# Performance work log

Measured on AMD Instinct MI355X. Metric: run time of the kernel, lower is better.

The kernel has to match this reference:

```python
import jax, jax.numpy as jnp
import numpy as np

B, S, H = 2, 512, 768
E, M, R, R2 = 64, 64, 128, 128
NER_C, REL_C, SIZE_E, CLS = 10, 8, 32, 101
NEG = -1e30


def _linear(x, w, b):
    # torch nn.Linear convention: w is [out, in]
    return x @ w.T + b


def _span_pool(emb, masks):
    # emb [B,S,H], masks [B,K,S] -> masked max over tokens -> [B,K,H]
    neg = jnp.where(masks[..., None] != 0, 0.0, NEG)  # [B,K,S,1]
    return jnp.max(neg + emb[:, None, :, :], axis=2)


def _classify_spans(input_ids, emb, masks, size_emb, rep_w, rep_b, head_w, head_b):
    pool = _span_pool(emb, masks)                      # [B,K,H]
    cls_idx = jnp.argmax((input_ids == CLS).astype(jnp.int32), axis=1)
    ctx = emb[jnp.arange(emb.shape[0]), cls_idx]       # [B,H] (get_token)
    rep = jnp.concatenate([jnp.broadcast_to(ctx[:, None, :], pool.shape), pool, size_emb], axis=-1)
    clf = _linear(jax.nn.relu(_linear(rep, rep_w, rep_b)), head_w, head_b)
    return clf, pool


def _classify_relations(pool, size_emb, rels, rel_masks, emb, w1, b1, w2, b2, w3, b3):
    Bc = pool.shape[0]
    bidx = jnp.arange(Bc)[:, None, None]
    pairs = pool[bidx, rels].reshape(Bc, rels.shape[1], -1)        # [B,R,2H]
    size_pairs = size_emb[bidx, rels].reshape(Bc, rels.shape[1], -1)  # [B,R,2*SIZE_E]
    # masked max over context tokens (rel mask)
    ctx = jnp.max(jnp.where(rel_masks[..., None] != 0, 0.0, NEG) + emb[:, None, :, :], axis=2)
    ctx = jnp.where(jnp.any(rel_masks != 0, axis=-1)[..., None], ctx, 0.0)
    rel_repr = jnp.concatenate([ctx, pairs, size_pairs], axis=-1)  # [B,R,3H+2*SIZE_E]
    h = jax.nn.relu(_linear(rel_repr, w1, b1))
    h = jax.nn.relu(_linear(h, w2, b2))
    return _linear(h, w3, b3)


def setup_inputs():
    key = jax.random.key(0)
    ks = jax.random.split(key, 24)
    p = lambda k, shape: jax.random.normal(k, shape, jnp.float32) * 0.02
    ids = jax.random.randint(ks[0], (B, S), 2000, 30000)
    ids = ids.at[:, 0].set(CLS)  # exactly one cls token per row
    return dict(
        input_ids=ids,
        entity_masks=jax.random.randint(ks[1], (B, E, S), 0, 2).astype(jnp.int32),
        entity_sizes=jax.random.randint(ks[2], (B, E), 0, 100),
        mention_masks=jax.random.randint(ks[3], (B, M, S), 0, 2).astype(jnp.int32),
        mention_sizes=jax.random.randint(ks[4], (B, M), 0, 100),
        relations=jax.random.randint(ks[5], (B, R, 2), 0, E),
        rel_masks=jax.random.randint(ks[6], (B, R, S), 0, 2).astype(jnp.int32),
        references=jax.random.randint(ks[7], (B, R2, 2), 0, M),
        references_masks=jax.random.randint(ks[8], (B, R2, S), 0, 2).astype(jnp.int32),
        token_embedding=jax.random.normal(ks[9], (B, S, H), jnp.float32),
        ner_size_emb=p(ks[10], (100, SIZE_E)),
        emd_size_emb=p(ks[11], (100, SIZE_E)),
        ner_rep_w=p(ks[12], (H, 2 * H + SIZE_E)), ner_rep_b=jnp.zeros(H, jnp.float32),
        ner_head_w=p(ks[13], (NER_C, H)), ner_head_b=jnp.zeros(NER_C, jnp.float32),
        emd_rep_w=p(ks[14], (H, 2 * H + SIZE_E)), emd_rep_b=jnp.zeros(H, jnp.float32),
        emd_head_w=p(ks[15], (2, H)), emd_head_b=jnp.zeros(2, jnp.float32),
        rel_w1=p(ks[16], (H, 3 * H + 2 * SIZE_E)), rel_b1=jnp.zeros(H, jnp.float32),
        rel_w2=p(ks[17], (H, H)), rel_b2=jnp.zeros(H, jnp.float32),
        rel_w3=p(ks[18], (REL_C, H)), rel_b3=jnp.zeros(REL_C, jnp.float32),
        cr_w1=p(ks[19], (H, 3 * H + 2 * SIZE_E)), cr_b1=jnp.zeros(H, jnp.float32),
        cr_w2=p(ks[20], (H, H)), cr_b2=jnp.zeros(H, jnp.float32),
        cr_w3=p(ks[21], (1, H)), cr_b3=jnp.zeros(1, jnp.float32),
    )


def reference(input_ids, entity_masks, entity_sizes, mention_masks, mention_sizes,
              relations, rel_masks, references, references_masks, token_embedding,
              ner_size_emb, emd_size_emb,
              ner_rep_w, ner_rep_b, ner_head_w, ner_head_b,
              emd_rep_w, emd_rep_b, emd_head_w, emd_head_b,
              rel_w1, rel_b1, rel_w2, rel_b2, rel_w3, rel_b3,
              cr_w1, cr_b1, cr_w2, cr_b2, cr_w3, cr_b3):
    sz = ner_size_emb[entity_sizes]                                    # [B,E,SIZE_E]
    entity_clf, entity_pool = _classify_spans(input_ids, token_embedding, entity_masks, sz,
                                              ner_rep_w, ner_rep_b, ner_head_w, ner_head_b)
    rel_clf = _classify_relations(entity_pool, sz, relations, rel_masks, token_embedding,
                                  rel_w1, rel_b1, rel_w2, rel_b2, rel_w3, rel_b3)
    msz = emd_size_emb[mention_sizes]
    mention_clf, mention_pool = _classify_spans(input_ids, token_embedding, mention_masks, msz,
                                                emd_rep_w, emd_rep_b, emd_head_w, emd_head_b)
    ref_clf = _classify_relations(mention_pool, msz, references, references_masks, token_embedding,
                                  cr_w1, cr_b1, cr_w2, cr_b2, cr_w3, cr_b3)
    return entity_clf, rel_clf, mention_clf, ref_clf
```

## Files before the change

### kernel.cpp

```cpp
#include <hip/hip_runtime.h>
#include <hip/hip_bf16.h>

typedef __hip_bfloat16 bf16;
typedef __attribute__((ext_vector_type(8))) short short8;
typedef __attribute__((ext_vector_type(4))) float f32x4;

#define SS 512
#define HD 768
#define NSPLIT 8

#define WOFF_NER 0
#define WOFF_EMD 1204224
#define WOFF_RW1 2408448
#define WOFF_CW1 4227072
#define WOFF_RW2 6045696
#define WOFF_CW2 6635520
#define W_TOT    7225344
#define CVT_BLOCKS (W_TOT / 4096)
#define D1_BLOCKS (768 + CVT_BLOCKS + 4)

__global__ __launch_bounds__(256) void k_d1(
    const int* __restrict__ e_masks, const int* __restrict__ m_masks,
    const int* __restrict__ r_masks, const int* __restrict__ c_masks,
    const float* __restrict__ emb, const int* __restrict__ input_ids,
    const int* __restrict__ esizes, const int* __restrict__ msizes,
    const float* __restrict__ nsemb, const float* __restrict__ esemb,
    const float* __restrict__ s0, const float* __restrict__ s1,
    const float* __restrict__ s2, const float* __restrict__ s3,
    const float* __restrict__ s4, const float* __restrict__ s5,
    bf16* __restrict__ wdst, bf16* __restrict__ part, int* __restrict__ flags,
    bf16* __restrict__ sze, bf16* __restrict__ szm,
    bf16* __restrict__ ctxb, float* __restrict__ out)
{
  int bx = blockIdx.x;
  int t  = threadIdx.x;

  if (bx >= 768 + CVT_BLOCKS) {
    int q = bx - (768 + CVT_BLOCKS);
    if (q == 0) {
      for (int i = t; i < 128 * 32; i += 256)
        sze[i] = __hip_bfloat16(nsemb[(size_t)esizes[i >> 5] * 32 + (i & 31)]);
    } else if (q == 1) {
      for (int i = t; i < 128 * 32; i += 256)
        szm[i] = __hip_bfloat16(esemb[(size_t)msizes[i >> 5] * 32 + (i & 31)]);
    } else if (q == 2) {
      __shared__ int s_cls;
      for (int b2 = 0; b2 < 2; b2++) {
        if (t == 0) s_cls = SS;
        __syncthreads();
        for (int s = t; s < SS; s += 256)
          if (input_ids[b2 * SS + s] == 101) atomicMin(&s_cls, s);
        __syncthreads();
        int ci = (s_cls == SS) ? 0 : s_cls;
        for (int hh = t; hh < HD; hh += 256)
          ctxb[(size_t)b2 * HD + hh] = __hip_bfloat16(emb[((size_t)b2 * SS + ci) * HD + hh]);
        __syncthreads();
      }
    } else {
      for (int i = t; i < 3840; i += 256) out[i] = 0.f;
    }
    return;
  }

  if (bx >= 768) {
    size_t i0 = (size_t)(bx - 768) * 4096;
    const float* s; size_t segoff;
    if      (i0 < WOFF_EMD) { s = s0; segoff = 0; }
    else if (i0 < WOFF_RW1) { s = s1; segoff = WOFF_EMD; }
    else if (i0 < WOFF_CW1) { s = s2; segoff = WOFF_RW1; }
    else if (i0 < WOFF_RW2) { s = s3; segoff = WOFF_CW1; }
    else if (i0 < WOFF_CW2) { s = s4; segoff = WOFF_RW2; }
    else                    { s = s5; segoff = WOFF_CW2; }
    #pragma unroll
    for (int j = 0; j < 4; j++) {
      size_t i = i0 + (size_t)j * 1024 + (size_t)t * 4;
      float4 v = *(const float4*)(s + (i - segoff));
      bf16 tmp[4] = { __hip_bfloat16(v.x), __hip_bfloat16(v.y),
                      __hip_bfloat16(v.z), __hip_bfloat16(v.w) };
      *(short4*)(wdst + i) = *(const short4*)tmp;
    }
    return;
  }

  int g  = bx % 48;
  int b  = (bx / 48) & 1;
  int sp = bx / 96;
  int j0 = g * 8;

  const int* marr; int row0;
  if      (j0 < 64)  { marr = e_masks; row0 = b*64  +  j0;        }
  else if (j0 < 128) { marr = m_masks; row0 = b*64  + (j0-64);    }
  else if (j0 < 256) { marr = r_masks; row0 = b*128 + (j0-128);   }
  else               { marr = c_masks; row0 = b*128 + (j0-256);   }

  __shared__ unsigned s_pack[64];
  __shared__ unsigned s_any;
  if (t == 0) s_any = 0u;
  __syncthreads();

  int sbase = sp * 64;
  if (t < 64) {
    unsigned w = 0;
    #pragma unroll
    for (int k = 0; k < 8; k++) {
      int mm = marr[(size_t)(row0 + k) * SS + sbase + t];
      w |= (mm != 0 ? 1u : 0u) << k;
    }
    s_pack[t] = w;
    atomicOr(&s_any, w);
  }
  __syncthreads();

  float acc[8][3];
  #pragma unroll
  for (int k = 0; k < 8; k++)
    #pragma unroll
    for (int i = 0; i < 3; i++) acc[k][i] = -INFINITY;

  const float* ep = emb + ((size_t)b * SS + sbase) * HD + t;
  #pragma unroll 2
  for (int s = 0; s < 64; s++) {
    float v0 = ep[0];
    float v1 = ep[256];
    float v2 = ep[512];
    ep += HD;
    unsigned wm = __builtin_amdgcn_readfirstlane(s_pack[s]);
    #pragma unroll
    for (int k = 0; k < 8; k++) {
      if (wm & (1u << k)) {
        acc[k][0] = fmaxf(acc[k][0], v0);
        acc[k][1] = fmaxf(acc[k][1], v1);
        acc[k][2] = fmaxf(acc[k][2], v2);
      }
    }
  }

  #pragma unroll
  for (int k = 0; k < 8; k++) {
    int sg = b * 384 + j0 + k;
    bf16* dst = part + ((size_t)sp * 768 + sg) * HD;
    dst[t]       = __hip_bfloat16(acc[k][0]);
    dst[t + 256] = __hip_bfloat16(acc[k][1]);
    dst[t + 512] = __hip_bfloat16(acc[k][2]);
  }
  if (t < 8) flags[sp * 768 + b * 384 + j0 + t] = (int)((s_any >> t) & 1u);
}

__global__ __launch_bounds__(256) void k_combine(
    const bf16* __restrict__ part, const int* __restrict__ flags,
    bf16* __restrict__ epool, bf16* __restrict__ mpool,
    bf16* __restrict__ rctx, bf16* __restrict__ cctx)
{
  int sg = blockIdx.x;
  int b = sg / 384, j = sg % 384;
  int any = 0;
  #pragma unroll
  for (int sp = 0; sp < NSPLIT; sp++) any |= flags[sp * 768 + sg];
  #pragma unroll
  for (int i = 0; i < 3; i++) {
    int h = threadIdx.x + i * 256;
    float v = -INFINITY;
    #pragma unroll
    for (int sp = 0; sp < NSPLIT; sp++)
      v = fmaxf(v, (float)part[((size_t)sp * 768 + sg) * HD + h]);
    if      (j < 64)  epool[((size_t)b*64  + j)       * HD + h] = __hip_bfloat16(v);
    else if (j < 128) mpool[((size_t)b*64  + (j-64))  * HD + h] = __hip_bfloat16(v);
    else if (j < 256) rctx [((size_t)b*128 + (j-128)) * HD + h] = __hip_bfloat16(any ? v : 0.f);
    else              cctx [((size_t)b*128 + (j-256)) * HD + h] = __hip_bfloat16(any ? v : 0.f);
  }
}

struct P1 {
  const bf16 *ctx, *pool, *sz; const int* ridx;
  const short* W; const float* bias;
  bf16* C;
  const float *hw, *hb; float* outp;
  int is_rel, N, K, Mtiles;
};
struct P1x4 { P1 p[4]; };

__global__ __launch_bounds__(256, 2) void k_gemm1(P1x4 args)
{
  P1 g = args.p[blockIdx.z];
  int x = blockIdx.x;
  if (x >= g.Mtiles) return;
  int mt = x * 32, nt = blockIdx.y * 32;
  int wave = threadIdx.x >> 6, lane = threadIdx.x & 63;
  int lm = lane & 15, quad = lane >> 4;
  int K_ = g.K;

  const bf16 *g0[2], *g1[2], *g2[2], *g3[2], *g4[2];
  int rr[2] = { mt + lm, mt + 16 + lm };
  #pragma unroll
  for (int i = 0; i < 2; i++) {
    int r = rr[i];
    if (g.is_rel) {
      int b = r >> 7;
      int i0 = g.ridx[2 * r], i1 = g.ridx[2 * r + 1];
      g0[i] = g.ctx  + (size_t)r * HD;
      g1[i] = g.pool + (size_t)(b * 64 + i0) * HD;
      g2[i] = g.pool + (size_t)(b * 64 + i1) * HD;
      g3[i] = g.sz   + (size_t)(b * 64 + i0) * 32;
      g4[i] = g.sz   + (size_t)(b * 64 + i1) * 32;
    } else {
      g0[i] = g.ctx  + (size_t)(r >> 6) * HD;
      g1[i] = g.pool + (size_t)r * HD;
      g2[i] = g.sz   + (size_t)r * 32;
      g3[i] = g2[i]; g4[i] = g2[i];
    }
  }
  const short* w0p = g.W + (size_t)(nt + lm)      * K_ + quad * 8;
  const short* w1p = g.W + (size_t)(nt + 16 + lm) * K_ + quad * 8;

  f32x4 acc00 = {0.f,0.f,0.f,0.f}, acc01 = {0.f,0.f,0.f,0.f};
  f32x4 acc10 = {0.f,0.f,0.f,0.f}, acc11 = {0.f,0.f,0.f,0.f};

  for (int k32 = wave * 32; k32 < K_; k32 += 128) {
    const bf16 *b0, *b1;
    if      (k32 < 768)  { b0 = g0[0] + k32;          b1 = g0[1] + k32;          }
    else if (k32 < 1536) { b0 = g1[0] + (k32 - 768);  b1 = g1[1] + (k32 - 768);  }
    else if (k32 < 2304) { b0 = g2[0] + (k32 - 1536); b1 = g2[1] + (k32 - 1536); }
    else if (k32 < 2336) { b0 = g3[0] + (k32 - 2304); b1 = g3[1] + (k32 - 2304); }
    else                 { b0 = g4[0] + (k32 - 2336); b1 = g4[1] + (k32 - 2336); }
    short8 a0 = *(const short8*)((const short*)b0 + quad * 8);
    short8 a1 = *(const short8*)((const short*)b1 + quad * 8);
    short8 w0 = *(const short8*)(w0p + k32);
    short8 w1 = *(const short8*)(w1p + k32);
    acc00 = __builtin_amdgcn_mfma_f32_16x16x32_bf16(a0, w0, acc00, 0, 0, 0);
    acc01 = __builtin_amdgcn_mfma_f32_16x16x32_bf16(a0, w1, acc01, 0, 0, 0);
    acc10 = __builtin_amdgcn_mfma_f32_16x16x32_bf16(a1, w0, acc10, 0, 0, 0);
    acc11 = __builtin_amdgcn_mfma_f32_16x16x32_bf16(a1, w1, acc11, 0, 0, 0);
  }

  __shared__ float smem[4 * 32 * 32];
  #pragma unroll
  for (int reg = 0; reg < 4; reg++) {
    int r = quad * 4 + reg;
    smem[wave*1024 + r*32 + lm]             = acc00[reg];
    smem[wave*1024 + r*32 + 16 + lm]        = acc01[reg];
    smem[wave*1024 + (16 + r)*32 + lm]      = acc10[reg];
    smem[wave*1024 + (16 + r)*32 + 16 + lm] = acc11[reg];
  }
  __syncthreads();

  int c = threadIdx.x & 31;
  int rb = threadIdx.x >> 5;
  float bb = g.bias[nt + c];
  #pragma unroll
  for (int i = 0; i < 4; i++) {
    int r = rb + 8 * i;
    float v = smem[r*32 + c] + smem[1024 + r*32 + c] + smem[2048 + r*32 + c] + smem[3072 + r*32 + c];
    v = fmaxf(v + bb, 0.f);
    if (g.C) g.C[(size_t)(mt + r) * HD + nt + c] = __hip_bfloat16(v);
    else     smem[r*32 + c] = v;
  }
  __syncthreads();

  if (!g.C) {
    int r = threadIdx.x >> 3, oi = threadIdx.x & 7;
    for (int o = oi; o < g.N; o += 8) {
      float s = 0.f;
      #pragma unroll
      for (int cc = 0; cc < 32; cc++) {
        int c2 = (cc + r) & 31;
        s += smem[r*32 + c2] * g.hw[(size_t)o * HD + nt + c2];
      }
      if (blockIdx.y == 0) s += g.hb[o];
      atomicAdd(g.outp + (size_t)(mt + r) * g.N + o, s);
    }
  }
}

struct P2 { const short* A; const short* W; const float* bias;
            const float *hw, *hb; float* outp; int N; };
struct P2x2 { P2 p[2]; };

__global__ __launch_bounds__(256, 2) void k_gemm2(P2x2 args)
{
  P2 g = args.p[blockIdx.z];
  int mt = blockIdx.x * 32, nt = blockIdx.y * 32;
  int wave = threadIdx.x >> 6, lane = threadIdx.x & 63;
  int lm = lane & 15, quad = lane >> 4;

  const short* a0p = g.A + (size_t)(mt + lm)      * HD + quad * 8;
  const short* a1p = g.A + (size_t)(mt + 16 + lm) * HD + quad * 8;
  const short* w0p = g.W + (size_t)(nt + lm)      * HD + quad * 8;
  const short* w1p = g.W + (size_t)(nt + 16 + lm) * HD + quad * 8;

  f32x4 acc00 = {0.f,0.f,0.f,0.f}, acc01 = {0.f,0.f,0.f,0.f};
  f32x4 acc10 = {0.f,0.f,0.f,0.f}, acc11 = {0.f,0.f,0.f,0.f};

  for (int k32 = wave * 32; k32 < HD; k32 += 128) {
    short8 a0 = *(const short8*)(a0p + k32);
    short8 a1 = *(const short8*)(a1p + k32);
    short8 w0 = *(const short8*)(w0p + k32);
    short8 w1 = *(const short8*)(w1p + k32);
    acc00 = __builtin_amdgcn_mfma_f32_16x16x32_bf16(a0, w0, acc00, 0, 0, 0);
    acc01 = __builtin_amdgcn_mfma_f32_16x16x32_bf16(a0, w1, acc01, 0, 0, 0);
    acc10 = __builtin_amdgcn_mfma_f32_16x16x32_bf16(a1, w0, acc10, 0, 0, 0);
    acc11 = __builtin_amdgcn_mfma_f32_16x16x32_bf16(a1, w1, acc11, 0, 0, 0);
  }

  __shared__ float smem[4 * 32 * 32];
  #pragma unroll
  for (int reg = 0; reg < 4; reg++) {
    int r = quad * 4 + reg;
    smem[wave*1024 + r*32 + lm]             = acc00[reg];
    smem[wave*1024 + r*32 + 16 + lm]        = acc01[reg];
    smem[wave*1024 + (16 + r)*32 + lm]      = acc10[reg];
    smem[wave*1024 + (16 + r)*32 + 16 + lm] = acc11[reg];
  }
  __syncthreads();

  int c = threadIdx.x & 31;
  int rb = threadIdx.x >> 5;
  float bb = g.bias[nt + c];
  #pragma unroll
  for (int i = 0; i < 4; i++) {
    int r = rb + 8 * i;
    float v = smem[r*32 + c] + smem[1024 + r*32 + c] + smem[2048 + r*32 + c] + smem[3072 + r*32 + c];
    smem[r*32 + c] = fmaxf(v + bb, 0.f);
  }
  __syncthreads();

  int r = threadIdx.x >> 3, oi = threadIdx.x & 7;
  for (int o = oi; o < g.N; o += 8) {
    float s = 0.f;
    #pragma unroll
    for (int cc = 0; cc < 32; cc++) {
      int c2 = (cc + r) & 31;
      s += smem[r*32 + c2] * g.hw[(size_t)o * HD + nt + c2];
    }
    if (blockIdx.y == 0) s += g.hb[o];
    atomicAdd(g.outp + (size_t)(mt + r) * g.N + o, s);
  }
}

extern "C" void kernel_launch(void* const* d_in, const int* in_sizes, int n_in,
                              void* d_out, int out_size, void* d_ws, size_t ws_size,
                              hipStream_t stream)
{
  const int*   input_ids  = (const int*)d_in[0];
  const int*   e_masks    = (const int*)d_in[1];
  const int*   e_sizes    = (const int*)d_in[2];
  const int*   m_masks    = (const int*)d_in[3];
  const int*   m_sizes    = (const int*)d_in[4];
  const int*   relations  = (const int*)d_in[5];
  const int*   r_masks    = (const int*)d_in[6];
  const int*   references = (const int*)d_in[7];
  const int*   c_masks    = (const int*)d_in[8];
  const float* emb        = (const float*)d_in[9];
  const float* nsemb      = (const float*)d_in[10];
  const float* esemb      = (const float*)d_in[11];
  const float* ner_rep_w  = (const float*)d_in[12];
  const float* ner_rep_b  = (const float*)d_in[13];
  const float* ner_head_w = (const float*)d_in[14];
  const float* ner_head_b = (const float*)d_in[15];
  const float* emd_rep_w  = (const float*)d_in[16];
  const float* emd_rep_b  = (const float*)d_in[17];
  const float* emd_head_w = (const float*)d_in[18];
  const float* emd_head_b = (const float*)d_in[19];
  const float* rel_w1 = (const float*)d_in[20];
  const float* rel_b1 = (const float*)d_in[21];
  const float* rel_w2 = (const float*)d_in[22];
  const float* rel_b2 = (const float*)d_in[23];
  const float* rel_w3 = (const float*)d_in[24];
  const float* rel_b3 = (const float*)d_in[25];
  const float* cr_w1 = (const float*)d_in[26];
  const float* cr_b1 = (const float*)d_in[27];
  const float* cr_w2 = (const float*)d_in[28];
  const float* cr_b2 = (const float*)d_in[29];
  const float* cr_w3 = (const float*)d_in[30];
  const float* cr_b3 = (const float*)d_in[31];
  float* out = (float*)d_out;

  bf16* wsb = (bf16*)d_ws;
  size_t ob = 0;
  bf16* WBF   = wsb + ob; ob += (size_t)W_TOT;
  bf16* PART  = wsb + ob; ob += (size_t)NSPLIT * 768 * HD;
  bf16* EPOOL = wsb + ob; ob += (size_t)128 * HD;
  bf16* MPOOL = wsb + ob; ob += (size_t)128 * HD;
  bf16* RCTX  = wsb + ob; ob += (size_t)256 * HD;
  bf16* CCTX  = wsb + ob; ob += (size_t)256 * HD;
  bf16* SZE   = wsb + ob; ob += (size_t)128 * 32;
  bf16* SZM   = wsb + ob; ob += (size_t)128 * 32;
  bf16* CTXB  = wsb + ob; ob += (size_t)2 * HD;
  bf16* RH1   = wsb + ob; ob += (size_t)256 * HD;
  bf16* CH1   = wsb + ob; ob += (size_t)256 * HD;
  int*  FLAGS = (int*)(wsb + ob); ob += (size_t)2 * NSPLIT * 768;

  k_d1<<<D1_BLOCKS, 256, 0, stream>>>(
      e_masks, m_masks, r_masks, c_masks, emb, input_ids,
      e_sizes, m_sizes, nsemb, esemb,
      ner_rep_w, emd_rep_w, rel_w1, cr_w1, rel_w2, cr_w2,
      WBF, PART, FLAGS, SZE, SZM, CTXB, out);

  k_combine<<<768, 256, 0, stream>>>(PART, FLAGS, EPOOL, MPOOL, RCTX, CCTX);

  P1x4 a1;
  a1.p[0] = { CTXB, EPOOL, SZE, nullptr,    (const short*)(WBF + WOFF_NER), ner_rep_b,
              nullptr, ner_head_w, ner_head_b, out,        0, 10, 1568, 4 };
  a1.p[1] = { CTXB, MPOOL, SZM, nullptr,    (const short*)(WBF + WOFF_EMD), emd_rep_b,
              nullptr, emd_head_w, emd_head_b, out + 3328, 0, 2,  1568, 4 };
  a1.p[2] = { RCTX, EPOOL, SZE, relations,  (const short*)(WBF + WOFF_RW1), rel_b1,
              RH1, nullptr, nullptr, nullptr,              1, 0,  2368, 8 };
  a1.p[3] = { CCTX, MPOOL, SZM, references, (const short*)(WBF + WOFF_CW1), cr_b1,
              CH1, nullptr, nullptr, nullptr,              1, 0,  2368, 8 };
  k_gemm1<<<dim3(8, 24, 4), 256, 0, stream>>>(a1);

  P2x2 a2;
  a2.p[0] = { (const short*)RH1, (const short*)(WBF + WOFF_RW2), rel_b2,
              rel_w3, rel_b3, out + 1280, 8 };
  a2.p[1] = { (const short*)CH1, (const short*)(WBF + WOFF_CW2), cr_b2,
              cr_w3, cr_b3, out + 3584, 1 };
  k_gemm2<<<dim3(8, 24, 2), 256, 0, stream>>>(a2);
}
```

Baseline: 220.9 us.

## Convert fp32 weights to bf16 inside GEMM loads and split pooling finer

Drops the separate pass that wrote bf16 copies of all weights to workspace. The GEMM kernels now read fp32 weights directly and convert them in registers before the MFMA. This removes one full weight read/write round trip, at the cost of reading twice the bytes in the GEMMs. The pooling pass doubles its token splits (16 splits of 32 tokens) and replaces the branchy max with a branchless add-and-max. It also gives each thread three contiguous hidden elements, which makes loads strided by 3 and less coalesced, and doubles the partial-buffer traffic in the combine step.

```diff
diff --git a/kernel.cpp b/kernel.cpp
--- a/kernel.cpp
+++ b/kernel.cpp
@@ -7,17 +7,21 @@
 
 #define SS 512
 #define HD 768
-#define NSPLIT 8
-
-#define WOFF_NER 0
-#define WOFF_EMD 1204224
-#define WOFF_RW1 2408448
-#define WOFF_CW1 4227072
-#define WOFF_RW2 6045696
-#define WOFF_CW2 6635520
-#define W_TOT    7225344
-#define CVT_BLOCKS (W_TOT / 4096)
-#define D1_BLOCKS (768 + CVT_BLOCKS + 4)
+#define NEGC (-1e30f)
+#define NSPLIT 16
+#define TOK 32
+#define POOL_BLOCKS 1536
+#define D1_BLOCKS (POOL_BLOCKS + 4)
+
+__device__ __forceinline__ short8 cvt8(float4 a, float4 b)
+{
+  union { bf16 h[8]; short8 s; } u;
+  u.h[0] = __hip_bfloat16(a.x); u.h[1] = __hip_bfloat16(a.y);
+  u.h[2] = __hip_bfloat16(a.z); u.h[3] = __hip_bfloat16(a.w);
+  u.h[4] = __hip_bfloat16(b.x); u.h[5] = __hip_bfloat16(b.y);
+  u.h[6] = __hip_bfloat16(b.z); u.h[7] = __hip_bfloat16(b.w);
+  return u.s;
+}
 
 __global__ __launch_bounds__(256) void k_d1(
     const int* __restrict__ e_masks, const int* __restrict__ m_masks,
@@ -25,18 +29,15 @@
     const float* __restrict__ emb, const int* __restrict__ input_ids,
     const int* __restrict__ esizes, const int* __restrict__ msizes,
     const float* __restrict__ nsemb, const float* __restrict__ esemb,
-    const float* __restrict__ s0, const float* __restrict__ s1,
-    const float* __restrict__ s2, const float* __restrict__ s3,
-    const float* __restrict__ s4, const float* __restrict__ s5,
-    bf16* __restrict__ wdst, bf16* __restrict__ part, int* __restrict__ flags,
+    bf16* __restrict__ part, int* __restrict__ flags,
     bf16* __restrict__ sze, bf16* __restrict__ szm,
     bf16* __restrict__ ctxb, float* __restrict__ out)
 {
   int bx = blockIdx.x;
   int t  = threadIdx.x;
 
-  if (bx >= 768 + CVT_BLOCKS) {
-    int q = bx - (768 + CVT_BLOCKS);
+  if (bx >= POOL_BLOCKS) {
+    int q = bx - POOL_BLOCKS;
     if (q == 0) {
       for (int i = t; i < 128 * 32; i += 256)
         sze[i] = __hip_bfloat16(nsemb[(size_t)esizes[i >> 5] * 32 + (i & 31)]);
@@ -62,26 +63,6 @@
     return;
   }
 
-  if (bx >= 768) {
-    size_t i0 = (size_t)(bx - 768) * 4096;
-    const float* s; size_t segoff;
-    if      (i0 < WOFF_EMD) { s = s0; segoff = 0; }
-    else if (i0 < WOFF_RW1) { s = s1; segoff = WOFF_EMD; }
-    else if (i0 < WOFF_CW1) { s = s2; segoff = WOFF_RW1; }
-    else if (i0 < WOFF_RW2) { s = s3; segoff = WOFF_CW1; }
-    else if (i0 < WOFF_CW2) { s = s4; segoff = WOFF_RW2; }
-    else                    { s = s5; segoff = WOFF_CW2; }
-    #pragma unroll
-    for (int j = 0; j < 4; j++) {
-      size_t i = i0 + (size_t)j * 1024 + (size_t)t * 4;
-      float4 v = *(const float4*)(s + (i - segoff));
-      bf16 tmp[4] = { __hip_bfloat16(v.x), __hip_bfloat16(v.y),
-                      __hip_bfloat16(v.z), __hip_bfloat16(v.w) };
-      *(short4*)(wdst + i) = *(const short4*)tmp;
-    }
-    return;
-  }
-
   int g  = bx % 48;
   int b  = (bx / 48) & 1;
   int sp = bx / 96;
@@ -93,13 +74,13 @@
   else if (j0 < 256) { marr = r_masks; row0 = b*128 + (j0-128);   }
   else               { marr = c_masks; row0 = b*128 + (j0-256);   }
 
-  __shared__ unsigned s_pack[64];
+  __shared__ unsigned s_pack[TOK];
   __shared__ unsigned s_any;
   if (t == 0) s_any = 0u;
   __syncthreads();
 
-  int sbase = sp * 64;
-  if (t < 64) {
+  int sbase = sp * TOK;
+  if (t < TOK) {
     unsigned w = 0;
     #pragma unroll
     for (int k = 0; k < 8; k++) {
@@ -111,37 +92,34 @@
   }
   __syncthreads();
 
-  float acc[8][3];
-  #pragma unroll
-  for (int k = 0; k < 8; k++)
-    #pragma unroll
-    for (int i = 0; i < 3; i++) acc[k][i] = -INFINITY;
-
-  const float* ep = emb + ((size_t)b * SS + sbase) * HD + t;
+  float a0[8], a1[8], a2[8];
+  #pragma unroll
+  for (int k = 0; k < 8; k++) { a0[k] = -INFINITY; a1[k] = -INFINITY; a2[k] = -INFINITY; }
+
+  const float* ep = emb + ((size_t)b * SS + sbase) * HD + t * 3;
   #pragma unroll 2
-  for (int s = 0; s < 64; s++) {
+  for (int s = 0; s < TOK; s++) {
     float v0 = ep[0];
-    float v1 = ep[256];
-    float v2 = ep[512];
+    float v1 = ep[1];
+    float v2 = ep[2];
     ep += HD;
-    unsigned wm = __builtin_amdgcn_readfirstlane(s_pack[s]);
+    unsigned wm = s_pack[s];
     #pragma unroll
     for (int k = 0; k < 8; k++) {
-      if (wm & (1u << k)) {
-        acc[k][0] = fmaxf(acc[k][0], v0);
-        acc[k][1] = fmaxf(acc[k][1], v1);
-        acc[k][2] = fmaxf(acc[k][2], v2);
-      }
+      float add = (wm & (1u << k)) ? 0.f : NEGC;
+      a0[k] = fmaxf(a0[k], v0 + add);
+      a1[k] = fmaxf(a1[k], v1 + add);
+      a2[k] = fmaxf(a2[k], v2 + add);
     }
   }
 
   #pragma unroll
   for (int k = 0; k < 8; k++) {
     int sg = b * 384 + j0 + k;
-    bf16* dst = part + ((size_t)sp * 768 + sg) * HD;
-    dst[t]       = __hip_bfloat16(acc[k][0]);
-    dst[t + 256] = __hip_bfloat16(acc[k][1]);
-    dst[t + 512] = __hip_bfloat16(acc[k][2]);
+    bf16* dst = part + ((size_t)sp * 768 + sg) * HD + t * 3;
+    dst[0] = __hip_bfloat16(a0[k]);
+    dst[1] = __hip_bfloat16(a1[k]);
+    dst[2] = __hip_bfloat16(a2[k]);
   }
   if (t < 8) flags[sp * 768 + b * 384 + j0 + t] = (int)((s_any >> t) & 1u);
 }
@@ -156,23 +134,31 @@
   int any = 0;
   #pragma unroll
   for (int sp = 0; sp < NSPLIT; sp++) any |= flags[sp * 768 + sg];
-  #pragma unroll
-  for (int i = 0; i < 3; i++) {
-    int h = threadIdx.x + i * 256;
-    float v = -INFINITY;
-    #pragma unroll
-    for (int sp = 0; sp < NSPLIT; sp++)
-      v = fmaxf(v, (float)part[((size_t)sp * 768 + sg) * HD + h]);
-    if      (j < 64)  epool[((size_t)b*64  + j)       * HD + h] = __hip_bfloat16(v);
-    else if (j < 128) mpool[((size_t)b*64  + (j-64))  * HD + h] = __hip_bfloat16(v);
-    else if (j < 256) rctx [((size_t)b*128 + (j-128)) * HD + h] = __hip_bfloat16(any ? v : 0.f);
-    else              cctx [((size_t)b*128 + (j-256)) * HD + h] = __hip_bfloat16(any ? v : 0.f);
-  }
+
+  int h = threadIdx.x * 3;
+  float v0 = -INFINITY, v1 = -INFINITY, v2 = -INFINITY;
+  #pragma unroll
+  for (int sp = 0; sp < NSPLIT; sp++) {
+    const bf16* src = part + ((size_t)sp * 768 + sg) * HD + h;
+    v0 = fmaxf(v0, (float)src[0]);
+    v1 = fmaxf(v1, (float)src[1]);
+    v2 = fmaxf(v2, (float)src[2]);
+  }
+  bf16* dst;
+  if      (j < 64)  { dst = epool + ((size_t)b*64  + j)       * HD + h; }
+  else if (j < 128) { dst = mpool + ((size_t)b*64  + (j-64))  * HD + h; }
+  else if (j < 256) { dst = rctx  + ((size_t)b*128 + (j-128)) * HD + h;
+                      if (!any) { v0 = 0.f; v1 = 0.f; v2 = 0.f; } }
+  else              { dst = cctx  + ((size_t)b*128 + (j-256)) * HD + h;
+                      if (!any) { v0 = 0.f; v1 = 0.f; v2 = 0.f; } }
+  dst[0] = __hip_bfloat16(v0);
+  dst[1] = __hip_bfloat16(v1);
+  dst[2] = __hip_bfloat16(v2);
 }
 
 struct P1 {
   const bf16 *ctx, *pool, *sz; const int* ridx;
-  const short* W; const float* bias;
+  const float* W; const float* bias;
   bf16* C;
   const float *hw, *hb; float* outp;
   int is_rel, N, K, Mtiles;
@@ -209,8 +195,8 @@
       g3[i] = g2[i]; g4[i] = g2[i];
     }
   }
-  const short* w0p = g.W + (size_t)(nt + lm)      * K_ + quad * 8;
-  const short* w1p = g.W + (size_t)(nt + 16 + lm) * K_ + quad * 8;
+  const float* w0p = g.W + (size_t)(nt + lm)      * K_ + quad * 8;
+  const float* w1p = g.W + (size_t)(nt + 16 + lm) * K_ + quad * 8;
 
   f32x4 acc00 = {0.f,0.f,0.f,0.f}, acc01 = {0.f,0.f,0.f,0.f};
   f32x4 acc10 = {0.f,0.f,0.f,0.f}, acc11 = {0.f,0.f,0.f,0.f};
@@ -224,8 +210,10 @@
     else                 { b0 = g4[0] + (k32 - 2336); b1 = g4[1] + (k32 - 2336); }
     short8 a0 = *(const short8*)((const short*)b0 + quad * 8);
     short8 a1 = *(const short8*)((const short*)b1 + quad * 8);
-    short8 w0 = *(const short8*)(w0p + k32);
-    short8 w1 = *(const short8*)(w1p + k32);
+    const float* wq0 = w0p + k32;
+    const float* wq1 = w1p + k32;
+    short8 w0 = cvt8(*(const float4*)wq0, *(const float4*)(wq0 + 4));
+    short8 w1 = cvt8(*(const float4*)wq1, *(const float4*)(wq1 + 4));
     acc00 = __builtin_amdgcn_mfma_f32_16x16x32_bf16(a0, w0, acc00, 0, 0, 0);
     acc01 = __builtin_amdgcn_mfma_f32_16x16x32_bf16(a0, w1, acc01, 0, 0, 0);
     acc10 = __builtin_amdgcn_mfma_f32_16x16x32_bf16(a1, w0, acc10, 0, 0, 0);
@@ -271,7 +259,7 @@
   }
 }
 
-struct P2 { const short* A; const short* W; const float* bias;
+struct P2 { const short* A; const float* W; const float* bias;
             const float *hw, *hb; float* outp; int N; };
 struct P2x2 { P2 p[2]; };
 
@@ -284,8 +272,8 @@
 
   const short* a0p = g.A + (size_t)(mt + lm)      * HD + quad * 8;
   const short* a1p = g.A + (size_t)(mt + 16 + lm) * HD + quad * 8;
-  const short* w0p = g.W + (size_t)(nt + lm)      * HD + quad * 8;
-  const short* w1p = g.W + (size_t)(nt + 16 + lm) * HD + quad * 8;
+  const float* w0p = g.W + (size_t)(nt + lm)      * HD + quad * 8;
+  const float* w1p = g.W + (size_t)(nt + 16 + lm) * HD + quad * 8;
 
   f32x4 acc00 = {0.f,0.f,0.f,0.f}, acc01 = {0.f,0.f,0.f,0.f};
   f32x4 acc10 = {0.f,0.f,0.f,0.f}, acc11 = {0.f,0.f,0.f,0.f};
@@ -293,8 +281,8 @@
   for (int k32 = wave * 32; k32 < HD; k32 += 128) {
     short8 a0 = *(const short8*)(a0p + k32);
     short8 a1 = *(const short8*)(a1p + k32);
-    short8 w0 = *(const short8*)(w0p + k32);
-    short8 w1 = *(const short8*)(w1p + k32);
+    short8 w0 = cvt8(*(const float4*)(w0p + k32), *(const float4*)(w0p + k32 + 4));
+    short8 w1 = cvt8(*(const float4*)(w1p + k32), *(const float4*)(w1p + k32 + 4));
     acc00 = __builtin_amdgcn_mfma_f32_16x16x32_bf16(a0, w0, acc00, 0, 0, 0);
     acc01 = __builtin_amdgcn_mfma_f32_16x16x32_bf16(a0, w1, acc01, 0, 0, 0);
     acc10 = __builtin_amdgcn_mfma_f32_16x16x32_bf16(a1, w0, acc10, 0, 0, 0);
@@ -376,7 +364,6 @@
 
   bf16* wsb = (bf16*)d_ws;
   size_t ob = 0;
-  bf16* WBF   = wsb + ob; ob += (size_t)W_TOT;
   bf16* PART  = wsb + ob; ob += (size_t)NSPLIT * 768 * HD;
   bf16* EPOOL = wsb + ob; ob += (size_t)128 * HD;
   bf16* MPOOL = wsb + ob; ob += (size_t)128 * HD;
@@ -392,26 +379,23 @@
   k_d1<<<D1_BLOCKS, 256, 0, stream>>>(
       e_masks, m_masks, r_masks, c_masks, emb, input_ids,
       e_sizes, m_sizes, nsemb, esemb,
-      ner_rep_w, emd_rep_w, rel_w1, cr_w1, rel_w2, cr_w2,
-      WBF, PART, FLAGS, SZE, SZM, CTXB, out);
+      PART, FLAGS, SZE, SZM, CTXB, out);
 
   k_combine<<<768, 256, 0, stream>>>(PART, FLAGS, EPOOL, MPOOL, RCTX, CCTX);
 
   P1x4 a1;
-  a1.p[0] = { CTXB, EPOOL, SZE, nullptr,    (const short*)(WBF + WOFF_NER), ner_rep_b,
+  a1.p[0] = { CTXB, EPOOL, SZE, nullptr,    ner_rep_w, ner_rep_b,
               nullptr, ner_head_w, ner_head_b, out,        0, 10, 1568, 4 };
-  a1.p[1] = { CTXB, MPOOL, SZM, nullptr,    (const short*)(WBF + WOFF_EMD), emd_rep_b,
+  a1.p[1] = { CTXB, MPOOL, SZM, nullptr,    emd_rep_w, emd_rep_b,
               nullptr, emd_head_w, emd_head_b, out + 3328, 0, 2,  1568, 4 };
-  a1.p[2] = { RCTX, EPOOL, SZE, relations,  (const short*)(WBF + WOFF_RW1), rel_b1,
+  a1.p[2] = { RCTX, EPOOL, SZE, relations,  rel_w1, rel_b1,
               RH1, nullptr, nullptr, nullptr,              1, 0,  2368, 8 };
-  a1.p[3] = { CCTX, MPOOL, SZM, references, (const short*)(WBF + WOFF_CW1), cr_b1,
+  a1.p[3] = { CCTX, MPOOL, SZM, references, cr_w1, cr_b1,
               CH1, nullptr, nullptr, nullptr,              1, 0,  2368, 8 };
   k_gemm1<<<dim3(8, 24, 4), 256, 0, stream>>>(a1);
 
   P2x2 a2;
-  a2.p[0] = { (const short*)RH1, (const short*)(WBF + WOFF_RW2), rel_b2,
-              rel_w3, rel_b3, out + 1280, 8 };
-  a2.p[1] = { (const short*)CH1, (const short*)(WBF + WOFF_CW2), cr_b2,
-              cr_w3, cr_b3, out + 3584, 1 };
+  a2.p[0] = { (const short*)RH1, rel_w2, rel_b2, rel_w3, rel_b3, out + 1280, 8 };
+  a2.p[1] = { (const short*)CH1, cr_w2,  cr_b2,  cr_w3,  cr_b3,  out + 3584, 1 };
   k_gemm2<<<dim3(8, 24, 2), 256, 0, stream>>>(a2);
 }
```

New measurement: 206.5 us. 1.07x faster.
